# Performance work log

Measured on AMD Instinct MI355X. Metric: run time of the kernel, lower is better.

Reference implementation:

```python
import jax, jax.numpy as jnp
import numpy as np

PAD_ID, SOS_ID, EOS_ID = 0, 1, 2


def setup_inputs() -> dict:
    key = jax.random.key(0)
    ks = jax.random.split(key, 8)
    V, E, H, B = 16000, 256, 512, 8
    s = 0.05  # weight scale to keep softmax well-conditioned
    return {
        "hidden": jax.random.normal(ks[0], (1, B, H), dtype=jnp.float32),
        "embedding": jax.random.normal(ks[1], (V, E), dtype=jnp.float32) * s,
        "w_ih": jax.random.normal(ks[2], (3 * H, E), dtype=jnp.float32) * s,
        "w_hh": jax.random.normal(ks[3], (3 * H, H), dtype=jnp.float32) * s,
        "b_ih": jax.random.normal(ks[4], (3 * H,), dtype=jnp.float32) * s,
        "b_hh": jax.random.normal(ks[5], (3 * H,), dtype=jnp.float32) * s,
        "w_out": jax.random.normal(ks[6], (V, H), dtype=jnp.float32) * s,
        "b_out": jax.random.normal(ks[7], (V,), dtype=jnp.float32) * s,
        "lenseq": 12,
        "k": 5,
    }


def reference(hidden, embedding, w_ih, w_hh, b_ih, b_hh, w_out, b_out, lenseq, k):
    V, E = embedding.shape
    _, B, H = hidden.shape
    dt = hidden.dtype
    pad_onehot = jax.nn.one_hot(PAD_ID, V, dtype=dt)

    def gru_cell(x_emb, h):  # x_emb: (k,B,E), h: (k,B,H); torch nn.GRU gate order r,z,n
        gi = x_emb @ w_ih.T + b_ih
        gh = h @ w_hh.T + b_hh
        i_r, i_z, i_n = jnp.split(gi, 3, axis=-1)
        h_r, h_z, h_n = jnp.split(gh, 3, axis=-1)
        r = jax.nn.sigmoid(i_r + h_r)
        z = jax.nn.sigmoid(i_z + h_z)
        n = jnp.tanh(i_n + r * h_n)
        return (1.0 - z) * n + z * h

    def step(carry, i):
        x, h, prob, res, _ = carry
        done = (x == EOS_ID) | (x == PAD_ID)            # (k,B)
        emb = embedding[x]                               # (k,B,E)
        h_new = gru_cell(emb, h)                         # (k,B,H)
        probs = jax.nn.softmax(h_new @ w_out.T + b_out, axis=-1)  # (k,B,V)
        pred = jnp.where(done[..., None], pad_onehot, probs)
        h = jnp.where(done[..., None], h, h_new)
        res = res.at[:, i].set(pred)                     # store raw pred (pre prob-scaling), as torch.cat copies
        scores = pred * prob[..., None]                  # (k,B,V); prob stays all-ones, faithful to source
        flat = scores.transpose(1, 0, 2).reshape(B, k * V)  # beam-major flatten per batch elem
        _, idx = jax.lax.top_k(flat, k)                  # (B,k)
        beam = (idx // V).T                              # (k,B)
        tok = (idx % V).T                                # (k,B)
        res = jnp.take_along_axis(res, beam[:, None, :, None], axis=0)
        prob = jnp.take_along_axis(prob, beam, axis=0)
        h = jnp.take_along_axis(h, beam[..., None], axis=0)
        return (tok, h, prob, res, pred), None

    x0 = jnp.full((k, B), SOS_ID, dtype=jnp.int32)
    h0 = jnp.broadcast_to(hidden[0], (k, B, H))
    prob0 = jnp.ones((k, B), dtype=dt)
    res0 = jnp.zeros((k, lenseq, B, V), dtype=dt)
    pred0 = jnp.zeros((k, B, V), dtype=dt)

    (x, h, prob, res, pred), _ = jax.lax.scan(step, (x0, h0, prob0, res0, pred0), jnp.arange(lenseq))

    # final top-1 selection per batch element over (k*V) flat scores
    scores = pred * prob[..., None]
    flat = scores.transpose(1, 0, 2).reshape(B, k * V)
    best_beam = jnp.argmax(flat, axis=-1) // V           # (B,)
    out = jnp.take_along_axis(res, best_beam[None, None, :, None], axis=0)[0]  # (lenseq,B,V)
    return out
```

## Files before the change

### kernel.cpp

```cpp
#include <hip/hip_runtime.h>

#define V 16000
#define E 256
#define H 512
#define HP 516
#define BB 8
#define T 12
#define NB 250
#define NBS 256
#define TPB 1024
#define CPB 64
#define BBH (BB * H)
#define AGENT __HIP_MEMORY_SCOPE_AGENT

typedef float vfloat4 __attribute__((ext_vector_type(4)));
typedef unsigned long long u64;


constexpr int W_FL   = CPB * 512;
constexpr int SH_OFF = W_FL;
constexpr int SP_OFF = SH_OFF + BB * HP;
constexpr int RS_OFF = SP_OFF + 64 * 48;
constexpr int RV_OFF = RS_OFF + 128;
constexpr int RI_OFF = RV_OFF + 128;
constexpr int SS_OFF = RI_OFF + 128;
constexpr int XN_OFF = SS_OFF + 8;
constexpr int X_OFF  = XN_OFF + 8;
constexpr int SMEM_FL = X_OFF + 8;
constexpr size_t SMEM_BYTES = (size_t)SMEM_FL * 4;

constexpr int CNT_LINES = 84;

__device__ __forceinline__ float dot4(float4 a, float4 b) {
    return a.x * b.x + a.y * b.y + a.z * b.z + a.w * b.w;
}

__global__ __launch_bounds__(256) void kinit(const float* __restrict__ hidden,
                                             float* __restrict__ hbuf,
                                             int* __restrict__ cnt) {
    int idx = blockIdx.x * 256 + threadIdx.x;
    if (idx < BBH) hbuf[idx] = hidden[idx];
    if (idx < CNT_LINES * 16) cnt[idx] = 0;
}

__device__ __forceinline__ void barA(int* __restrict__ cnt, int ep) {
    __syncthreads();
    if (blockIdx.x < 64 && threadIdx.x == 0)
        __hip_atomic_fetch_add(&cnt[(64 + (blockIdx.x >> 2)) * 16], 1,
                               __ATOMIC_RELEASE, AGENT);
    if (blockIdx.x == 0) {
        if (threadIdx.x < 16) {
            while (__hip_atomic_load(&cnt[(64 + threadIdx.x) * 16],
                                     __ATOMIC_RELAXED, AGENT) < 4 * ep)
                __builtin_amdgcn_s_sleep(1);
        }
        __syncthreads();
        if (threadIdx.x == 0)
            __hip_atomic_store(&cnt[63 * 16], ep, __ATOMIC_RELAXED, AGENT);
    } else {
        if (threadIdx.x == 0) {
            while (__hip_atomic_load(&cnt[63 * 16], __ATOMIC_RELAXED, AGENT) < ep)
                __builtin_amdgcn_s_sleep(1);
        }
    }
    __builtin_amdgcn_fence(__ATOMIC_ACQUIRE, "workgroup");
    __syncthreads();
}

__device__ __forceinline__ void barB(int* __restrict__ cnt, int ep) {
    __syncthreads();
    if (threadIdx.x == 0) {
        int g = blockIdx.x >> 2;
        __hip_atomic_fetch_add(&cnt[g * 16], 1, __ATOMIC_RELEASE, AGENT);
    }
    if (blockIdx.x == 0) {
        if (threadIdx.x < 63) {
            int expct = (threadIdx.x == 62) ? 2 : 4;
            while (__hip_atomic_load(&cnt[threadIdx.x * 16],
                                     __ATOMIC_RELAXED, AGENT) < expct * ep)
                __builtin_amdgcn_s_sleep(1);
        }
        __syncthreads();
        if (threadIdx.x == 0)
            __hip_atomic_store(&cnt[80 * 16], ep, __ATOMIC_RELAXED, AGENT);
    } else {
        if (threadIdx.x == 0) {
            while (__hip_atomic_load(&cnt[80 * 16], __ATOMIC_RELAXED, AGENT) < ep)
                __builtin_amdgcn_s_sleep(1);
        }
    }
    __builtin_amdgcn_fence(__ATOMIC_ACQUIRE, "workgroup");
    __syncthreads();
}

__global__ __launch_bounds__(TPB, 4) void kmain(
    const float* __restrict__ emb_tab,
    const float* __restrict__ w_ih,
    const float* __restrict__ w_hh,
    const float* __restrict__ b_ih,
    const float* __restrict__ b_hh,
    const float* __restrict__ w_out,
    const float* __restrict__ b_out,
    float* __restrict__ hbuf,
    u64* __restrict__ pqm,
    int* __restrict__ pqi,
    int* __restrict__ cnt,
    float* __restrict__ out)
{
    extern __shared__ float smem[];
    float* w_lds  = smem;
    float* s_h    = smem + SH_OFF;
    float* s_part = smem + SP_OFF;
    float* s_e    = smem + SP_OFF;
    float* s_rsum = smem + RS_OFF;
    float* s_rval = smem + RV_OFF;
    int*   s_ridx = (int*)(smem + RI_OFF);
    float* s_S    = smem + SS_OFF;
    int*   s_Xn   = (int*)(smem + XN_OFF);
    int*   s_X    = (int*)(smem + X_OFF);

    const int blk = blockIdx.x, tid = threadIdx.x;

    for (int i = tid; i < CPB * 128; i += TPB) {
        int col = i >> 7;
        int q4  = (i & 127) << 2;
        int vv  = blk * CPB + col;
        float4 w4 = *(const float4*)(w_out + (size_t)vv * H + q4);
        int sw = q4 ^ ((col & 7) << 2) ^ (((q4 >> 5) & 7) << 2);
        *(float4*)(w_lds + col * 512 + sw) = w4;
    }
    if (tid < BB) s_X[tid] = 1;
    __syncthreads();

    const int lane = tid & 63;
    const int wv   = tid >> 6;
    const int rh   = lane & 3;
    const int kq   = (lane >> 2) & 15;
    const int rowhalf = wv & 1;
    const int cs   = wv >> 1;
    const int r    = rowhalf * 4 + rh;
    const int xw   = (cs ^ (kq & 7)) << 2;
    const int hswz = (kq & 7) << 2;

    float bo[8];
#pragma unroll
    for (int p = 0; p < 8; p++) bo[p] = b_out[blk * CPB + p * 8 + cs];

    for (int t = 0; t < T; t++) {
        const float* h_cur = hbuf + (size_t)t * BBH;
        float*       h_nxt = hbuf + (size_t)(t + 1) * BBH;

        if (blk < 64) {
            int hr = tid >> 7, k4 = (tid & 127) << 2;
            const u64* p = (const u64*)(h_cur + hr * H + k4);
            union { u64 u; float f[2]; } c0, c1;
            c0.u = __hip_atomic_load(p,     __ATOMIC_RELAXED, AGENT);
            c1.u = __hip_atomic_load(p + 1, __ATOMIC_RELAXED, AGENT);
            *(float4*)(s_h + hr * HP + k4) =
                make_float4(c0.f[0], c0.f[1], c1.f[0], c1.f[1]);
        }
        __syncthreads();
        if (blk < 64 && tid < 512) {
            const int jl = tid >> 6;
            const int ar = (tid >> 3) & 7;
            const int kq8 = tid & 7;
            const int j  = blk * 8 + jl;
            const int pair = jl * 8 + ar;
            float gir = 0.f, giz = 0.f, gin = 0.f, ghr = 0.f, ghz = 0.f, ghn = 0.f;
            {
                const float* erow = emb_tab + (size_t)s_X[ar] * E;
                const float* w0 = w_ih + (size_t)j * E;
                const float* w1 = w0 + (size_t)H * E;
                const float* w2 = w1 + (size_t)H * E;
                const int k0 = kq8 * (E / 8);
                for (int k = 0; k < E / 8; k += 4) {
                    float4 ev = *(const float4*)(erow + k0 + k);
                    gir += dot4(*(const float4*)(w0 + k0 + k), ev);
                    giz += dot4(*(const float4*)(w1 + k0 + k), ev);
                    gin += dot4(*(const float4*)(w2 + k0 + k), ev);
                }
            }
            {
                const float* hrow = s_h + ar * HP;
                const float* w0 = w_hh + (size_t)j * H;
                const float* w1 = w0 + (size_t)H * H;
                const float* w2 = w1 + (size_t)H * H;
                const int k0 = kq8 * (H / 8);
                for (int k = 0; k < H / 8; k += 4) {
                    float4 hv = *(const float4*)(hrow + k0 + k);
                    ghr += dot4(*(const float4*)(w0 + k0 + k), hv);
                    ghz += dot4(*(const float4*)(w1 + k0 + k), hv);
                    ghn += dot4(*(const float4*)(w2 + k0 + k), hv);
                }
            }
            float* sp = s_part + pair * 48;
            sp[0 * 8 + kq8] = gir; sp[1 * 8 + kq8] = giz; sp[2 * 8 + kq8] = gin;
            sp[3 * 8 + kq8] = ghr; sp[4 * 8 + kq8] = ghz; sp[5 * 8 + kq8] = ghn;
        }
        __syncthreads();
        if (blk < 64 && tid < 512 && (tid & 7) == 0) {
            const int pair = (tid >> 6) * 8 + ((tid >> 3) & 7);
            const int jl = pair >> 3, ar = pair & 7;
            const int j  = blk * 8 + jl;
            const float* sp2 = s_part + pair * 48;
            float G[6];
#pragma unroll
            for (int gg = 0; gg < 6; gg++) {
                float s = 0.f;
#pragma unroll
                for (int q = 0; q < 8; q++) s += sp2[gg * 8 + q];
                G[gg] = s;
            }
            float ir  = G[0] + b_ih[j],         hr_ = G[3] + b_hh[j];
            float iz  = G[1] + b_ih[H + j],     hz  = G[4] + b_hh[H + j];
            float inn = G[2] + b_ih[2 * H + j], hn  = G[5] + b_hh[2 * H + j];
            float rg = 1.f / (1.f + __expf(-(ir + hr_)));
            float zg = 1.f / (1.f + __expf(-(iz + hz)));
            float ng = tanhf(inn + rg * hn);
            float ho = s_h[ar * HP + j];
            int xr = s_X[ar];
            bool dn = (xr == 0) || (xr == 2);
            float hv = dn ? ho : ((1.f - zg) * ng + zg * ho);
            s_rsum[ar * 8 + jl] = hv;
        }
        __syncthreads();
        if (blk < 64 && tid < 32) {
            int ar = tid >> 2, q2 = (tid & 3) << 1;
            union { float f[2]; u64 u; } pk;
            pk.f[0] = s_rsum[ar * 8 + q2];
            pk.f[1] = s_rsum[ar * 8 + q2 + 1];
            __hip_atomic_store((u64*)(h_nxt + (size_t)ar * H + blk * 8 + q2),
                               pk.u, __ATOMIC_RELAXED, AGENT);
        }
        barA(cnt, t + 1);

        {
            int hr = tid >> 7, k4 = (tid & 127) << 2;
            const u64* p = (const u64*)(h_nxt + hr * H + k4);
            union { u64 u; float f[2]; } c0, c1;
            c0.u = __hip_atomic_load(p,     __ATOMIC_RELAXED, AGENT);
            c1.u = __hip_atomic_load(p + 1, __ATOMIC_RELAXED, AGENT);
            int sw = k4 ^ (((k4 >> 5) & 7) << 2);
            *(float4*)(s_h + hr * HP + sw) =
                make_float4(c0.f[0], c0.f[1], c1.f[0], c1.f[1]);
        }
        __syncthreads();
        {
            float4 hreg[8];
            const float* hb = s_h + r * HP + kq * 32;
#pragma unroll
            for (int i = 0; i < 8; i++)
                hreg[i] = *(const float4*)(hb + ((4 * i) ^ hswz));

            float s_acc = 0.f, bv = -1.f; int bi = 0x7fffffff;
#pragma unroll
            for (int p = 0; p < 8; p++) {
                const int col = p * 8 + cs;
                const int vv  = blk * CPB + col;
                const float* wb = w_lds + col * 512 + kq * 32;
                float acc = 0.f;
#pragma unroll
                for (int i = 0; i < 8; i++) {
                    float4 w4 = *(const float4*)(wb + ((4 * i) ^ xw));
                    acc += dot4(w4, hreg[i]);
                }
                acc += __shfl_xor(acc, 4, 64);
                acc += __shfl_xor(acc, 8, 64);
                acc += __shfl_xor(acc, 16, 64);
                acc += __shfl_xor(acc, 32, 64);
                float ee = __expf(acc + bo[p]);
                if (kq == 0) s_e[r * 65 + col] = ee;
                s_acc += ee;
                if (ee > bv) { bv = ee; bi = vv; }
            }
            if (kq == 0) {
                s_rsum[wv * 8 + r] = s_acc;
                s_rval[wv * 8 + r] = bv;
                s_ridx[wv * 8 + r] = bi;
            } else if (kq == 1) {
                int ro = (1 - rowhalf) * 4 + rh;
                s_rsum[wv * 8 + ro] = 0.f;
                s_rval[wv * 8 + ro] = -1.f;
                s_ridx[wv * 8 + ro] = 0x7fffffff;
            }
        }
        __syncthreads();
        if (tid < 64) {
            float s  = s_rsum[tid] + s_rsum[tid + 64];
            float av = s_rval[tid], bv2 = s_rval[tid + 64];
            int   ai = s_ridx[tid], bi2 = s_ridx[tid + 64];
            float bv = av; int bi = ai;
            if (bv2 > bv || (bv2 == bv && bi2 < bi)) { bv = bv2; bi = bi2; }
#pragma unroll
            for (int m = 8; m <= 32; m <<= 1) {
                s += __shfl_xor(s, m, 64);
                float ov = __shfl_xor(bv, m, 64);
                int   oi = __shfl_xor(bi, m, 64);
                if (ov > bv || (ov == bv && oi < bi)) { bv = ov; bi = oi; }
            }
            if (tid < 8) {
                union { float f[2]; u64 u; } pk;
                pk.f[0] = s; pk.f[1] = bv;
                size_t o = (size_t)(t * 8 + tid) * NBS + blk;
                __hip_atomic_store(&pqm[o], pk.u, __ATOMIC_RELAXED, AGENT);
                __hip_atomic_store(&pqi[o], bi,   __ATOMIC_RELAXED, AGENT);
            }
        }
        barB(cnt, t + 1);

        if (wv < 8) {
            const size_t base = (size_t)(t * 8 + wv) * NBS;
            float s = 0.f, bv = -1.f; int bi = 0x7fffffff;
#pragma unroll
            for (int c = 0; c < 4; c++) {
                int idx = lane + 64 * c;
                if (idx < NB) {
                    union { float f[2]; u64 u; } pk;
                    pk.u = __hip_atomic_load(&pqm[base + idx],
                                             __ATOMIC_RELAXED, AGENT);
                    s += pk.f[0];
                    float ov = pk.f[1];
                    int   oi = __hip_atomic_load(&pqi[base + idx],
                                                 __ATOMIC_RELAXED, AGENT);
                    if (ov > bv || (ov == bv && oi < bi)) { bv = ov; bi = oi; }
                }
            }
            for (int m = 1; m < 64; m <<= 1) {
                s += __shfl_xor(s, m, 64);
                float ov = __shfl_xor(bv, m, 64);
                int   oi = __shfl_xor(bi, m, 64);
                if (ov > bv || (ov == bv && oi < bi)) { bv = ov; bi = oi; }
            }
            if (lane == 0) { s_S[wv] = s; s_Xn[wv] = bi; }
        }
        __syncthreads();
        {
            float* out_t = out + (size_t)t * BB * V;
            if (tid < 128) {
                int row = tid >> 4;
                int c4  = (tid & 15) << 2;
                int xr = s_X[row];
                bool dn = (xr == 0) || (xr == 2);
                float inv = 1.f / s_S[row];
                int vbase = blk * CPB + c4;
                vfloat4 o4;
                o4.x = dn ? ((vbase + 0 == 0) ? 1.f : 0.f) : s_e[row * 65 + c4 + 0] * inv;
                o4.y = dn ? ((vbase + 1 == 0) ? 1.f : 0.f) : s_e[row * 65 + c4 + 1] * inv;
                o4.z = dn ? ((vbase + 2 == 0) ? 1.f : 0.f) : s_e[row * 65 + c4 + 2] * inv;
                o4.w = dn ? ((vbase + 3 == 0) ? 1.f : 0.f) : s_e[row * 65 + c4 + 3] * inv;
                __builtin_nontemporal_store(o4,
                    (vfloat4*)(out_t + (size_t)row * V + vbase));
            }
        }
        __syncthreads();
        if (tid < 8) {
            int xo = s_X[tid];
            s_X[tid] = ((xo == 0) || (xo == 2)) ? 0 : s_Xn[tid];
        }
        __syncthreads();
    }
}

extern "C" void kernel_launch(void* const* d_in, const int* in_sizes, int n_in,
                              void* d_out, int out_size, void* d_ws, size_t ws_size,
                              hipStream_t stream) {
    (void)in_sizes; (void)n_in; (void)out_size; (void)ws_size;
    const float* hidden    = (const float*)d_in[0];
    const float* embedding = (const float*)d_in[1];
    const float* w_ih      = (const float*)d_in[2];
    const float* w_hh      = (const float*)d_in[3];
    const float* b_ih      = (const float*)d_in[4];
    const float* b_hh      = (const float*)d_in[5];
    const float* w_out     = (const float*)d_in[6];
    const float* b_out     = (const float*)d_in[7];
    float* out = (float*)d_out;

    float* ws    = (float*)d_ws;
    float* hbuf  = ws;
    u64*   pqm   = (u64*)(hbuf + (size_t)(T + 1) * BBH);
    int*   pqi   = (int*)(pqm + (size_t)T * 8 * NBS);
    int*   cnt   = pqi + (size_t)T * 8 * NBS;

    hipFuncSetAttribute((const void*)kmain,
        hipFuncAttributeMaxDynamicSharedMemorySize,
        (int)SMEM_BYTES);

    kinit<<<16, 256, 0, stream>>>(hidden, hbuf, cnt);
    kmain<<<NB, TPB, SMEM_BYTES, stream>>>(embedding, w_ih, w_hh, b_ih, b_hh,
                                           w_out, b_out, hbuf, pqm, pqi,
                                           cnt, out);
}
```

Before: 558.6 us.

## Spread barrier release flags and pack tagged partials into 16-byte records

The single global release flag in both grid barriers becomes eight flags on separate cache lines, each block polls the one chosen by its index, and waiters sleep longer between polls. This is meant to reduce contention on one hot line. The per-block sum/max/index partials are merged into one 16-byte record carrying a launch-and-step tag. Readers use a single vector load and fall back to atomic loads only when the tag does not match. The tag comes from a per-launch counter seeded with a timer value, which adds some complexity and relies on the tag check to detect stale data.

```diff
diff --git a/kernel.cpp b/kernel.cpp
--- a/kernel.cpp
+++ b/kernel.cpp
@@ -26,10 +26,11 @@
 constexpr int SS_OFF = RI_OFF + 128;
 constexpr int XN_OFF = SS_OFF + 8;
 constexpr int X_OFF  = XN_OFF + 8;
-constexpr int SMEM_FL = X_OFF + 8;
+constexpr int DC_OFF = X_OFF + 8;
+constexpr int SMEM_FL = DC_OFF + 1;
 constexpr size_t SMEM_BYTES = (size_t)SMEM_FL * 4;
 
-constexpr int CNT_LINES = 84;
+constexpr int CNT_LINES = 100;
 
 __device__ __forceinline__ float dot4(float4 a, float4 b) {
     return a.x * b.x + a.y * b.y + a.z * b.z + a.w * b.w;
@@ -37,10 +38,17 @@
 
 __global__ __launch_bounds__(256) void kinit(const float* __restrict__ hidden,
                                              float* __restrict__ hbuf,
-                                             int* __restrict__ cnt) {
+                                             int* __restrict__ cnt,
+                                             int* __restrict__ dct) {
     int idx = blockIdx.x * 256 + threadIdx.x;
     if (idx < BBH) hbuf[idx] = hidden[idx];
     if (idx < CNT_LINES * 16) cnt[idx] = 0;
+    if (blockIdx.x == 0 && threadIdx.x == 0) {
+        int old = __hip_atomic_load(dct, __ATOMIC_RELAXED, AGENT);
+        int tk  = (int)(__builtin_amdgcn_s_memtime() >> 6);
+        __hip_atomic_store(dct, old + ((tk | 1) & 0xFFFF),
+                           __ATOMIC_RELAXED, AGENT);
+    }
 }
 
 __device__ __forceinline__ void barA(int* __restrict__ cnt, int ep) {
@@ -55,12 +63,14 @@
                 __builtin_amdgcn_s_sleep(1);
         }
         __syncthreads();
-        if (threadIdx.x == 0)
-            __hip_atomic_store(&cnt[63 * 16], ep, __ATOMIC_RELAXED, AGENT);
+        if (threadIdx.x < 8)
+            __hip_atomic_store(&cnt[(84 + threadIdx.x) * 16], ep,
+                               __ATOMIC_RELAXED, AGENT);
     } else {
         if (threadIdx.x == 0) {
-            while (__hip_atomic_load(&cnt[63 * 16], __ATOMIC_RELAXED, AGENT) < ep)
-                __builtin_amdgcn_s_sleep(1);
+            while (__hip_atomic_load(&cnt[(84 + (blockIdx.x & 7)) * 16],
+                                     __ATOMIC_RELAXED, AGENT) < ep)
+                __builtin_amdgcn_s_sleep(4);
         }
     }
     __builtin_amdgcn_fence(__ATOMIC_ACQUIRE, "workgroup");
@@ -81,12 +91,14 @@
                 __builtin_amdgcn_s_sleep(1);
         }
         __syncthreads();
-        if (threadIdx.x == 0)
-            __hip_atomic_store(&cnt[80 * 16], ep, __ATOMIC_RELAXED, AGENT);
+        if (threadIdx.x < 8)
+            __hip_atomic_store(&cnt[(92 + threadIdx.x) * 16], ep,
+                               __ATOMIC_RELAXED, AGENT);
     } else {
         if (threadIdx.x == 0) {
-            while (__hip_atomic_load(&cnt[80 * 16], __ATOMIC_RELAXED, AGENT) < ep)
-                __builtin_amdgcn_s_sleep(1);
+            while (__hip_atomic_load(&cnt[(92 + (blockIdx.x & 7)) * 16],
+                                     __ATOMIC_RELAXED, AGENT) < ep)
+                __builtin_amdgcn_s_sleep(4);
         }
     }
     __builtin_amdgcn_fence(__ATOMIC_ACQUIRE, "workgroup");
@@ -102,9 +114,9 @@
     const float* __restrict__ w_out,
     const float* __restrict__ b_out,
     float* __restrict__ hbuf,
-    u64* __restrict__ pqm,
-    int* __restrict__ pqi,
+    vfloat4* __restrict__ pq,
     int* __restrict__ cnt,
+    int* __restrict__ dct,
     float* __restrict__ out)
 {
     extern __shared__ float smem[];
@@ -118,6 +130,7 @@
     float* s_S    = smem + SS_OFF;
     int*   s_Xn   = (int*)(smem + XN_OFF);
     int*   s_X    = (int*)(smem + X_OFF);
+    int*   s_dct  = (int*)(smem + DC_OFF);
 
     const int blk = blockIdx.x, tid = threadIdx.x;
 
@@ -130,7 +143,10 @@
         *(float4*)(w_lds + col * 512 + sw) = w4;
     }
     if (tid < BB) s_X[tid] = 1;
+    if (tid == 0)
+        *s_dct = __hip_atomic_load(dct, __ATOMIC_RELAXED, AGENT);
     __syncthreads();
+    const int tagbase = (*s_dct) << 4;
 
     const int lane = tid & 63;
     const int wv   = tid >> 6;
@@ -149,6 +165,7 @@
     for (int t = 0; t < T; t++) {
         const float* h_cur = hbuf + (size_t)t * BBH;
         float*       h_nxt = hbuf + (size_t)(t + 1) * BBH;
+        const int tagv = tagbase | (t + 1);
 
         if (blk < 64) {
             int hr = tid >> 7, k4 = (tid & 127) << 2;
@@ -299,30 +316,39 @@
                 if (ov > bv || (ov == bv && oi < bi)) { bv = ov; bi = oi; }
             }
             if (tid < 8) {
-                union { float f[2]; u64 u; } pk;
-                pk.f[0] = s; pk.f[1] = bv;
-                size_t o = (size_t)(t * 8 + tid) * NBS + blk;
-                __hip_atomic_store(&pqm[o], pk.u, __ATOMIC_RELAXED, AGENT);
-                __hip_atomic_store(&pqi[o], bi,   __ATOMIC_RELAXED, AGENT);
+                u64* pp = (u64*)(pq + (size_t)(t * 8 + tid) * NBS + blk);
+                union { float f[2]; u64 u; } lo;
+                lo.f[0] = s; lo.f[1] = bv;
+                __hip_atomic_store(pp, lo.u, __ATOMIC_RELAXED, AGENT);
+                u64 hi = (u64)(unsigned)bi | ((u64)(unsigned)tagv << 32);
+                __hip_atomic_store(pp + 1, hi, __ATOMIC_RELEASE, AGENT);
             }
         }
         barB(cnt, t + 1);
 
         if (wv < 8) {
-            const size_t base = (size_t)(t * 8 + wv) * NBS;
+            const vfloat4* pqt = pq + (size_t)(t * 8 + wv) * NBS;
             float s = 0.f, bv = -1.f; int bi = 0x7fffffff;
 #pragma unroll
             for (int c = 0; c < 4; c++) {
                 int idx = lane + 64 * c;
                 if (idx < NB) {
-                    union { float f[2]; u64 u; } pk;
-                    pk.u = __hip_atomic_load(&pqm[base + idx],
-                                             __ATOMIC_RELAXED, AGENT);
-                    s += pk.f[0];
-                    float ov = pk.f[1];
-                    int   oi = __hip_atomic_load(&pqi[base + idx],
-                                                 __ATOMIC_RELAXED, AGENT);
-                    if (ov > bv || (ov == bv && oi < bi)) { bv = ov; bi = oi; }
+                    vfloat4 q = pqt[idx];
+                    float qs, qv; int qi;
+                    if (__float_as_uint(q.w) == (unsigned)tagv) {
+                        qs = q.x; qv = q.y;
+                        qi = (int)__float_as_uint(q.z);
+                    } else {
+                        const u64* pp = (const u64*)(pqt + idx);
+                        union { u64 u; float f[2]; } lo;
+                        lo.u = __hip_atomic_load(pp, __ATOMIC_RELAXED, AGENT);
+                        u64 hi = __hip_atomic_load(pp + 1,
+                                                   __ATOMIC_RELAXED, AGENT);
+                        qs = lo.f[0]; qv = lo.f[1];
+                        qi = (int)(unsigned)(hi & 0xFFFFFFFFu);
+                    }
+                    s += qs;
+                    if (qv > bv || (qv == bv && qi < bi)) { bv = qv; bi = qi; }
                 }
             }
             for (int m = 1; m < 64; m <<= 1) {
@@ -375,18 +401,18 @@
     const float* b_out     = (const float*)d_in[7];
     float* out = (float*)d_out;
 
-    float* ws    = (float*)d_ws;
-    float* hbuf  = ws;
-    u64*   pqm   = (u64*)(hbuf + (size_t)(T + 1) * BBH);
-    int*   pqi   = (int*)(pqm + (size_t)T * 8 * NBS);
-    int*   cnt   = pqi + (size_t)T * 8 * NBS;
+    float* ws      = (float*)d_ws;
+    float* hbuf    = ws;
+    vfloat4* pq    = (vfloat4*)(hbuf + (size_t)(T + 1) * BBH);
+    int*   cnt     = (int*)(pq + (size_t)T * 8 * NBS);
+    int*   dct     = cnt + CNT_LINES * 16;
 
     hipFuncSetAttribute((const void*)kmain,
         hipFuncAttributeMaxDynamicSharedMemorySize,
         (int)SMEM_BYTES);
 
-    kinit<<<16, 256, 0, stream>>>(hidden, hbuf, cnt);
+    kinit<<<16, 256, 0, stream>>>(hidden, hbuf, cnt, dct);
     kmain<<<NB, TPB, SMEM_BYTES, stream>>>(embedding, w_ih, w_hh, b_ih, b_hh,
-                                           w_out, b_out, hbuf, pqm, pqi,
-                                           cnt, out);
-}
+                                           w_out, b_out, hbuf, pq,
+                                           cnt, dct, out);
+}
```

Result: slower. 590.8 us (+5.8%).

## Replace grid barrier with per-slot epoch-tagged flags for partial reductions

Applied to the files above, without the earlier changes.

Removes the second grid-wide barrier (barB) after blocks publish per-row softmax partial sums and argmax candidates. Each block now writes a 16-byte slot holding sum, max, index and the step epoch, storing the epoch half with release semantics. Reader waves spin on each slot until its epoch matches instead of waiting on a centralized counter. This trades one global barrier round-trip for distributed polling on 250 slots per row, and adds a zero-initialization pass over the slot array in the init kernel.

```diff
diff --git a/kernel.cpp b/kernel.cpp
--- a/kernel.cpp
+++ b/kernel.cpp
@@ -37,10 +37,13 @@
 
 __global__ __launch_bounds__(256) void kinit(const float* __restrict__ hidden,
                                              float* __restrict__ hbuf,
-                                             int* __restrict__ cnt) {
+                                             int* __restrict__ cnt,
+                                             vfloat4* __restrict__ pq) {
     int idx = blockIdx.x * 256 + threadIdx.x;
     if (idx < BBH) hbuf[idx] = hidden[idx];
     if (idx < CNT_LINES * 16) cnt[idx] = 0;
+    for (int i = idx; i < T * 8 * NBS; i += 16 * 256)
+        pq[i] = (vfloat4){0.f, 0.f, 0.f, 0.f};
 }
 
 __device__ __forceinline__ void barA(int* __restrict__ cnt, int ep) {
@@ -67,32 +70,6 @@
     __syncthreads();
 }
 
-__device__ __forceinline__ void barB(int* __restrict__ cnt, int ep) {
-    __syncthreads();
-    if (threadIdx.x == 0) {
-        int g = blockIdx.x >> 2;
-        __hip_atomic_fetch_add(&cnt[g * 16], 1, __ATOMIC_RELEASE, AGENT);
-    }
-    if (blockIdx.x == 0) {
-        if (threadIdx.x < 63) {
-            int expct = (threadIdx.x == 62) ? 2 : 4;
-            while (__hip_atomic_load(&cnt[threadIdx.x * 16],
-                                     __ATOMIC_RELAXED, AGENT) < expct * ep)
-                __builtin_amdgcn_s_sleep(1);
-        }
-        __syncthreads();
-        if (threadIdx.x == 0)
-            __hip_atomic_store(&cnt[80 * 16], ep, __ATOMIC_RELAXED, AGENT);
-    } else {
-        if (threadIdx.x == 0) {
-            while (__hip_atomic_load(&cnt[80 * 16], __ATOMIC_RELAXED, AGENT) < ep)
-                __builtin_amdgcn_s_sleep(1);
-        }
-    }
-    __builtin_amdgcn_fence(__ATOMIC_ACQUIRE, "workgroup");
-    __syncthreads();
-}
-
 __global__ __launch_bounds__(TPB, 4) void kmain(
     const float* __restrict__ emb_tab,
     const float* __restrict__ w_ih,
@@ -102,8 +79,7 @@
     const float* __restrict__ w_out,
     const float* __restrict__ b_out,
     float* __restrict__ hbuf,
-    u64* __restrict__ pqm,
-    int* __restrict__ pqi,
+    vfloat4* __restrict__ pq,
     int* __restrict__ cnt,
     float* __restrict__ out)
 {
@@ -299,29 +275,33 @@
                 if (ov > bv || (ov == bv && oi < bi)) { bv = ov; bi = oi; }
             }
             if (tid < 8) {
-                union { float f[2]; u64 u; } pk;
-                pk.f[0] = s; pk.f[1] = bv;
-                size_t o = (size_t)(t * 8 + tid) * NBS + blk;
-                __hip_atomic_store(&pqm[o], pk.u, __ATOMIC_RELAXED, AGENT);
-                __hip_atomic_store(&pqi[o], bi,   __ATOMIC_RELAXED, AGENT);
-            }
-        }
-        barB(cnt, t + 1);
+                u64* pp = (u64*)(pq + (size_t)(t * 8 + tid) * NBS + blk);
+                union { float f[2]; u64 u; } lo;
+                lo.f[0] = s; lo.f[1] = bv;
+                __hip_atomic_store(pp, lo.u, __ATOMIC_RELAXED, AGENT);
+                u64 hi = (u64)(unsigned)bi | ((u64)(unsigned)(t + 1) << 32);
+                __hip_atomic_store(pp + 1, hi, __ATOMIC_RELEASE, AGENT);
+            }
+        }
 
         if (wv < 8) {
-            const size_t base = (size_t)(t * 8 + wv) * NBS;
+            const vfloat4* pqt = pq + (size_t)(t * 8 + wv) * NBS;
             float s = 0.f, bv = -1.f; int bi = 0x7fffffff;
 #pragma unroll
             for (int c = 0; c < 4; c++) {
                 int idx = lane + 64 * c;
                 if (idx < NB) {
-                    union { float f[2]; u64 u; } pk;
-                    pk.u = __hip_atomic_load(&pqm[base + idx],
-                                             __ATOMIC_RELAXED, AGENT);
-                    s += pk.f[0];
-                    float ov = pk.f[1];
-                    int   oi = __hip_atomic_load(&pqi[base + idx],
-                                                 __ATOMIC_RELAXED, AGENT);
+                    const u64* pp = (const u64*)(pqt + idx);
+                    u64 hi = __hip_atomic_load(pp + 1, __ATOMIC_RELAXED, AGENT);
+                    while ((unsigned)(hi >> 32) != (unsigned)(t + 1)) {
+                        __builtin_amdgcn_s_sleep(1);
+                        hi = __hip_atomic_load(pp + 1, __ATOMIC_RELAXED, AGENT);
+                    }
+                    union { u64 u; float f[2]; } lo;
+                    lo.u = __hip_atomic_load(pp, __ATOMIC_RELAXED, AGENT);
+                    s += lo.f[0];
+                    float ov = lo.f[1];
+                    int   oi = (int)(unsigned)(hi & 0xFFFFFFFFu);
                     if (ov > bv || (ov == bv && oi < bi)) { bv = ov; bi = oi; }
                 }
             }
@@ -375,18 +355,17 @@
     const float* b_out     = (const float*)d_in[7];
     float* out = (float*)d_out;
 
-    float* ws    = (float*)d_ws;
-    float* hbuf  = ws;
-    u64*   pqm   = (u64*)(hbuf + (size_t)(T + 1) * BBH);
-    int*   pqi   = (int*)(pqm + (size_t)T * 8 * NBS);
-    int*   cnt   = pqi + (size_t)T * 8 * NBS;
+    float* ws      = (float*)d_ws;
+    float* hbuf    = ws;
+    vfloat4* pq    = (vfloat4*)(hbuf + (size_t)(T + 1) * BBH);
+    int*   cnt     = (int*)(pq + (size_t)T * 8 * NBS);
 
     hipFuncSetAttribute((const void*)kmain,
         hipFuncAttributeMaxDynamicSharedMemorySize,
         (int)SMEM_BYTES);
 
-    kinit<<<16, 256, 0, stream>>>(hidden, hbuf, cnt);
+    kinit<<<16, 256, 0, stream>>>(hidden, hbuf, cnt, pq);
     kmain<<<NB, TPB, SMEM_BYTES, stream>>>(embedding, w_ih, w_hh, b_ih, b_hh,
-                                           w_out, b_out, hbuf, pqm, pqi,
+                                           w_out, b_out, hbuf, pq,
                                            cnt, out);
 }
```

Result: slower. 648.0 us (+16.0%).
